# Kernel optimization log

Measured on AMD Instinct MI355X. Metric: run time of the kernel, lower is better.

Reference implementation:

```python
import jax, jax.numpy as jnp
import numpy as np

IN_F, OUT_F = 64, 32
N = IN_F * OUT_F + OUT_F  # 2080 sampled parameters (weights + bias)
B, S = 8, 2048
SCALE_INIT = 1.0 * float(np.sqrt(2.0 / (IN_F + OUT_F)))


def setup_inputs() -> dict:
    key = jax.random.key(0)
    k_x, k_eps, k_loc, k_cov = jax.random.split(key, 4)
    x = jax.random.normal(k_x, (B, S, IN_F), dtype=jnp.float32)
    eps = jax.random.normal(k_eps, (B, S, N), dtype=jnp.float32)
    loc = 0.01 * jax.random.normal(k_loc, (N,), dtype=jnp.float32)
    logvar = jnp.full((N,), float(np.log(SCALE_INIT)), dtype=jnp.float32)
    n_off = N * (N - 1) // 2
    cov_flat = 0.001 * jax.random.normal(k_cov, (n_off,), dtype=jnp.float32)
    return {"x": x, "eps": eps, "loc": loc, "logvar": logvar, "cov_flat": cov_flat}


def reference(x, eps, loc, logvar, cov_flat):
    n = loc.shape[0]
    in_f = x.shape[-1]
    out_f = n // (in_f + 1)  # n = out*(in+1)
    # flat_to_triangular (strictly lower) + make_cholesky, vectorized scatter
    rows, cols = np.tril_indices(n, -1)
    A = jnp.zeros((n, n), dtype=x.dtype).at[rows, cols].set(cov_flat)
    L = A + jnp.diag(jnp.exp(logvar * 0.5))  # off-diag from cov, diag = std
    # MultivariateNormal rsample: loc + L @ eps (per batch sample)
    W = loc + jnp.einsum('bsn,mn->bsm', eps, L)  # [B,S,N]
    b = W[..., :out_f]
    Wm = W[..., out_f:].reshape(*W.shape[:-1], in_f, out_f)  # [B,S,in,out]
    y = jnp.einsum('bsh,bshk->bsk', x, Wm) + b
    return y
```

## Files before the change

### kernel.cpp

```cpp
#include <hip/hip_runtime.h>
#include <hip/hip_bf16.h>

#define IN_F  64
#define OUT_F 32
#define NV    2080
#define NPAD  2176
#define MM    16384
#define KK    2080

typedef __attribute__((ext_vector_type(4))) float f32x4;
typedef __bf16 bf16x8 __attribute__((ext_vector_type(8)));

using gas_ptr = const __attribute__((address_space(1))) void*;
using lds_ptr = __attribute__((address_space(3))) void*;

__global__ __launch_bounds__(256) void build_L_k(const float* __restrict__ cov,
                                                 const float* __restrict__ logvar,
                                                 __hip_bfloat16* __restrict__ LB) {
    const int idx = blockIdx.x * 256 + threadIdx.x;
    const int m = idx / KK;
    const int k = idx - m * KK;
    float v = 0.0f;
    if (m < NV) {
        if (k < m)       v = cov[(size_t)(m * (m - 1) / 2) + k];
        else if (k == m) v = expf(0.5f * logvar[m]);
    }
    LB[idx] = __float2bfloat16(v);
}

__global__ __launch_bounds__(256) void cvt_bf16_k(const float4* __restrict__ in,
                                                  uint4* __restrict__ out) {
    const size_t i = (size_t)blockIdx.x * 256 + threadIdx.x;
    float4 a = in[2 * i];
    float4 b = in[2 * i + 1];
    union { uint4 u; __hip_bfloat16 h[8]; } o;
    o.h[0] = __float2bfloat16(a.x); o.h[1] = __float2bfloat16(a.y);
    o.h[2] = __float2bfloat16(a.z); o.h[3] = __float2bfloat16(a.w);
    o.h[4] = __float2bfloat16(b.x); o.h[5] = __float2bfloat16(b.y);
    o.h[6] = __float2bfloat16(b.z); o.h[7] = __float2bfloat16(b.w);
    out[i] = o.u;
}

__global__ __launch_bounds__(256) void gemm_zl_k(const __hip_bfloat16* __restrict__ A,
                                                 const __hip_bfloat16* __restrict__ BT,
                                                 __hip_bfloat16* __restrict__ Z) {
    __shared__ __align__(16) __hip_bfloat16 As[2][128 * 32];
    __shared__ __align__(16) __hip_bfloat16 Bs[2][128 * 32];

    const int tid  = threadIdx.x;
    const int bm   = blockIdx.x;
    const int bn   = 16 - blockIdx.y;
    const int wave = tid >> 6;
    const int lane = tid & 63;
    const int wr   = wave >> 1;
    const int wc   = wave & 1;
    const int quad = lane >> 4;
    const int r16  = lane & 15;

    const int kblocks = min(KK / 32, 4 * bn + 4);

    const __hip_bfloat16* Ag = A  + (size_t)bm * 128 * KK;
    const __hip_bfloat16* Bg = BT + (size_t)bn * 128 * KK;

    const int c0 = tid, c1 = tid + 256;
    const int ar0 = c0 >> 2, ap0 = (c0 & 3) ^ ((ar0 >> 1) & 3);
    const int ar1 = c1 >> 2, ap1 = (c1 & 3) ^ ((ar1 >> 1) & 3);
    const size_t gofs0 = (size_t)ar0 * KK + ap0 * 8;
    const size_t gofs1 = (size_t)ar1 * KK + ap1 * 8;

    f32x4 acc[4][4];
#pragma unroll
    for (int i = 0; i < 4; i++)
#pragma unroll
        for (int j = 0; j < 4; j++) acc[i][j] = f32x4{0.f, 0.f, 0.f, 0.f};

    int aofs[4], bofs[4];
#pragma unroll
    for (int i = 0; i < 4; i++) {
        const int arow = 64 * wr + 16 * i + r16;
        aofs[i] = arow * 32 + (quad ^ ((arow >> 1) & 3)) * 8;
        const int brow = 64 * wc + 16 * i + r16;
        bofs[i] = brow * 32 + (quad ^ ((brow >> 1) & 3)) * 8;
    }

    __builtin_amdgcn_global_load_lds((gas_ptr)(Ag + gofs0), (lds_ptr)(&As[0][0] + c0 * 8), 16, 0, 0);
    __builtin_amdgcn_global_load_lds((gas_ptr)(Ag + gofs1), (lds_ptr)(&As[0][0] + c1 * 8), 16, 0, 0);
    __builtin_amdgcn_global_load_lds((gas_ptr)(Bg + gofs0), (lds_ptr)(&Bs[0][0] + c0 * 8), 16, 0, 0);
    __builtin_amdgcn_global_load_lds((gas_ptr)(Bg + gofs1), (lds_ptr)(&Bs[0][0] + c1 * 8), 16, 0, 0);

    for (int kb = 0; kb < kblocks; ++kb) {
        const int cur = kb & 1;
        __syncthreads();

        if (kb + 1 < kblocks) {
            const size_t k0 = (size_t)(kb + 1) * 32;
            __builtin_amdgcn_global_load_lds((gas_ptr)(Ag + k0 + gofs0), (lds_ptr)(&As[cur ^ 1][0] + c0 * 8), 16, 0, 0);
            __builtin_amdgcn_global_load_lds((gas_ptr)(Ag + k0 + gofs1), (lds_ptr)(&As[cur ^ 1][0] + c1 * 8), 16, 0, 0);
            __builtin_amdgcn_global_load_lds((gas_ptr)(Bg + k0 + gofs0), (lds_ptr)(&Bs[cur ^ 1][0] + c0 * 8), 16, 0, 0);
            __builtin_amdgcn_global_load_lds((gas_ptr)(Bg + k0 + gofs1), (lds_ptr)(&Bs[cur ^ 1][0] + c1 * 8), 16, 0, 0);
        }

        bf16x8 af[4], bfr[4];
#pragma unroll
        for (int i = 0; i < 4; i++) af[i]  = *(const bf16x8*)(&As[cur][0] + aofs[i]);
#pragma unroll
        for (int j = 0; j < 4; j++) bfr[j] = *(const bf16x8*)(&Bs[cur][0] + bofs[j]);
#pragma unroll
        for (int i = 0; i < 4; i++)
#pragma unroll
            for (int j = 0; j < 4; j++)
                acc[i][j] = __builtin_amdgcn_mfma_f32_16x16x32_bf16(af[i], bfr[j], acc[i][j], 0, 0, 0);
    }

#pragma unroll
    for (int i = 0; i < 4; i++) {
#pragma unroll
        for (int j = 0; j < 4; j++) {
            const int row0 = bm * 128 + 64 * wr + 16 * i + quad * 4;
            const int col  = bn * 128 + 64 * wc + 16 * j + r16;
#pragma unroll
            for (int r = 0; r < 4; r++)
                Z[(size_t)(row0 + r) * NPAD + col] = __float2bfloat16(acc[i][j][r]);
        }
    }
}

__global__ __launch_bounds__(256) void epilogue_k(const __hip_bfloat16* __restrict__ Z,
                                                  const float* __restrict__ x,
                                                  const float* __restrict__ loc,
                                                  float* __restrict__ y) {
    __shared__ float locs[NV];
    __shared__ float xs[8][IN_F];
    const int tid = threadIdx.x;
    const int t0  = blockIdx.x * 8;
    for (int i = tid; i < NV; i += 256) locs[i] = loc[i];
    {
        int i = tid;
        xs[i >> 6][i & 63] = x[(size_t)(t0 + (i >> 6)) * IN_F + (i & 63)];
        i += 256;
        xs[i >> 6][i & 63] = x[(size_t)(t0 + (i >> 6)) * IN_F + (i & 63)];
    }
    __syncthreads();

    const int k  = tid & 31;
    const int tl = tid >> 5;
    const size_t t = (size_t)t0 + tl;
    const __hip_bfloat16* zr = Z + t * NPAD;

    float sum = locs[k] + __bfloat162float(zr[k]);
#pragma unroll 8
    for (int h = 0; h < IN_F; ++h) {
        const int m = OUT_F + (h << 5) + k;
        sum += xs[tl][h] * (locs[m] + __bfloat162float(zr[m]));
    }
    y[t * OUT_F + k] = sum;
}

extern "C" void kernel_launch(void* const* d_in, const int* in_sizes, int n_in,
                              void* d_out, int out_size, void* d_ws, size_t ws_size,
                              hipStream_t stream) {
    const float* x      = (const float*)d_in[0];
    const float* eps    = (const float*)d_in[1];
    const float* loc    = (const float*)d_in[2];
    const float* logvar = (const float*)d_in[3];
    const float* cov    = (const float*)d_in[4];
    float* y = (float*)d_out;

    char* ws = (char*)d_ws;
    __hip_bfloat16* EpsB = (__hip_bfloat16*)ws;
    __hip_bfloat16* LB   = (__hip_bfloat16*)(ws + (size_t)MM * KK * 2);
    __hip_bfloat16* Zb   = (__hip_bfloat16*)(ws + (size_t)MM * KK * 2
                                                + (size_t)NPAD * KK * 2);

    build_L_k<<<(NPAD * KK) / 256, 256, 0, stream>>>(cov, logvar, LB);
    cvt_bf16_k<<<(MM * KK / 8) / 256, 256, 0, stream>>>((const float4*)eps, (uint4*)EpsB);
    gemm_zl_k<<<dim3(MM / 128, NPAD / 128), 256, 0, stream>>>(EpsB, LB, Zb);
    epilogue_k<<<MM / 8, 256, 0, stream>>>(Zb, x, loc, y);
}
```

Baseline: 338.2 us.

## Fuse eps bf16 conversion into GEMM loads and fold loc into GEMM epilogue

Removes the separate fp32-to-bf16 conversion pass over eps: the GEMM now streams fp32 eps tiles straight into LDS with a new XOR swizzle and converts them to bf16 while building MFMA fragments. The loc bias is added in the GEMM store, and the epilogue kernel is rewritten to stage each Z row in LDS with one wave per token and a shuffle reduction. This avoids writing and re-reading a large bf16 copy of eps, at the cost of double the A-tile LDS footprint, more global bytes per GEMM k-step, and conversion ALU work inside the MFMA loop.

```diff
diff --git a/kernel.cpp b/kernel.cpp
--- a/kernel.cpp
+++ b/kernel.cpp
@@ -28,23 +28,11 @@
     LB[idx] = __float2bfloat16(v);
 }
 
-__global__ __launch_bounds__(256) void cvt_bf16_k(const float4* __restrict__ in,
-                                                  uint4* __restrict__ out) {
-    const size_t i = (size_t)blockIdx.x * 256 + threadIdx.x;
-    float4 a = in[2 * i];
-    float4 b = in[2 * i + 1];
-    union { uint4 u; __hip_bfloat16 h[8]; } o;
-    o.h[0] = __float2bfloat16(a.x); o.h[1] = __float2bfloat16(a.y);
-    o.h[2] = __float2bfloat16(a.z); o.h[3] = __float2bfloat16(a.w);
-    o.h[4] = __float2bfloat16(b.x); o.h[5] = __float2bfloat16(b.y);
-    o.h[6] = __float2bfloat16(b.z); o.h[7] = __float2bfloat16(b.w);
-    out[i] = o.u;
-}
-
-__global__ __launch_bounds__(256) void gemm_zl_k(const __hip_bfloat16* __restrict__ A,
+__global__ __launch_bounds__(256) void gemm_zl_k(const float* __restrict__ A,
                                                  const __hip_bfloat16* __restrict__ BT,
+                                                 const float* __restrict__ loc,
                                                  __hip_bfloat16* __restrict__ Z) {
-    __shared__ __align__(16) __hip_bfloat16 As[2][128 * 32];
+    __shared__ __align__(16) float          As[2][128 * 32];
     __shared__ __align__(16) __hip_bfloat16 Bs[2][128 * 32];
 
     const int tid  = threadIdx.x;
@@ -59,14 +47,24 @@
 
     const int kblocks = min(KK / 32, 4 * bn + 4);
 
-    const __hip_bfloat16* Ag = A  + (size_t)bm * 128 * KK;
+    const float*          Ag = A  + (size_t)bm * 128 * KK;
     const __hip_bfloat16* Bg = BT + (size_t)bn * 128 * KK;
 
+    int aldsofs[4];
+    size_t agofs[4];
+#pragma unroll
+    for (int i = 0; i < 4; i++) {
+        const int c   = tid + 256 * i;
+        const int row = c >> 3;
+        const int pg  = (c & 7) ^ (row & 7);
+        aldsofs[i] = c * 4;
+        agofs[i]   = (size_t)row * KK + pg * 4;
+    }
     const int c0 = tid, c1 = tid + 256;
-    const int ar0 = c0 >> 2, ap0 = (c0 & 3) ^ ((ar0 >> 1) & 3);
-    const int ar1 = c1 >> 2, ap1 = (c1 & 3) ^ ((ar1 >> 1) & 3);
-    const size_t gofs0 = (size_t)ar0 * KK + ap0 * 8;
-    const size_t gofs1 = (size_t)ar1 * KK + ap1 * 8;
+    const int br0 = c0 >> 2, bp0 = (c0 & 3) ^ ((br0 >> 1) & 3);
+    const int br1 = c1 >> 2, bp1 = (c1 & 3) ^ ((br1 >> 1) & 3);
+    const size_t bgofs0 = (size_t)br0 * KK + bp0 * 8;
+    const size_t bgofs1 = (size_t)br1 * KK + bp1 * 8;
 
     f32x4 acc[4][4];
 #pragma unroll
@@ -74,19 +72,23 @@
 #pragma unroll
         for (int j = 0; j < 4; j++) acc[i][j] = f32x4{0.f, 0.f, 0.f, 0.f};
 
-    int aofs[4], bofs[4];
+    int aofs0[4], aofs1[4], bofs[4];
 #pragma unroll
     for (int i = 0; i < 4; i++) {
         const int arow = 64 * wr + 16 * i + r16;
-        aofs[i] = arow * 32 + (quad ^ ((arow >> 1) & 3)) * 8;
+        const int s0 = (2 * quad) ^ (arow & 7);
+        const int s1 = (2 * quad + 1) ^ (arow & 7);
+        aofs0[i] = arow * 32 + s0 * 4;
+        aofs1[i] = arow * 32 + s1 * 4;
         const int brow = 64 * wc + 16 * i + r16;
         bofs[i] = brow * 32 + (quad ^ ((brow >> 1) & 3)) * 8;
     }
 
-    __builtin_amdgcn_global_load_lds((gas_ptr)(Ag + gofs0), (lds_ptr)(&As[0][0] + c0 * 8), 16, 0, 0);
-    __builtin_amdgcn_global_load_lds((gas_ptr)(Ag + gofs1), (lds_ptr)(&As[0][0] + c1 * 8), 16, 0, 0);
-    __builtin_amdgcn_global_load_lds((gas_ptr)(Bg + gofs0), (lds_ptr)(&Bs[0][0] + c0 * 8), 16, 0, 0);
-    __builtin_amdgcn_global_load_lds((gas_ptr)(Bg + gofs1), (lds_ptr)(&Bs[0][0] + c1 * 8), 16, 0, 0);
+#pragma unroll
+    for (int i = 0; i < 4; i++)
+        __builtin_amdgcn_global_load_lds((gas_ptr)(Ag + agofs[i]), (lds_ptr)(&As[0][0] + aldsofs[i]), 16, 0, 0);
+    __builtin_amdgcn_global_load_lds((gas_ptr)(Bg + bgofs0), (lds_ptr)(&Bs[0][0] + c0 * 8), 16, 0, 0);
+    __builtin_amdgcn_global_load_lds((gas_ptr)(Bg + bgofs1), (lds_ptr)(&Bs[0][0] + c1 * 8), 16, 0, 0);
 
     for (int kb = 0; kb < kblocks; ++kb) {
         const int cur = kb & 1;
@@ -94,15 +96,24 @@
 
         if (kb + 1 < kblocks) {
             const size_t k0 = (size_t)(kb + 1) * 32;
-            __builtin_amdgcn_global_load_lds((gas_ptr)(Ag + k0 + gofs0), (lds_ptr)(&As[cur ^ 1][0] + c0 * 8), 16, 0, 0);
-            __builtin_amdgcn_global_load_lds((gas_ptr)(Ag + k0 + gofs1), (lds_ptr)(&As[cur ^ 1][0] + c1 * 8), 16, 0, 0);
-            __builtin_amdgcn_global_load_lds((gas_ptr)(Bg + k0 + gofs0), (lds_ptr)(&Bs[cur ^ 1][0] + c0 * 8), 16, 0, 0);
-            __builtin_amdgcn_global_load_lds((gas_ptr)(Bg + k0 + gofs1), (lds_ptr)(&Bs[cur ^ 1][0] + c1 * 8), 16, 0, 0);
+#pragma unroll
+            for (int i = 0; i < 4; i++)
+                __builtin_amdgcn_global_load_lds((gas_ptr)(Ag + k0 + agofs[i]),
+                                                 (lds_ptr)(&As[cur ^ 1][0] + aldsofs[i]), 16, 0, 0);
+            __builtin_amdgcn_global_load_lds((gas_ptr)(Bg + k0 + bgofs0), (lds_ptr)(&Bs[cur ^ 1][0] + c0 * 8), 16, 0, 0);
+            __builtin_amdgcn_global_load_lds((gas_ptr)(Bg + k0 + bgofs1), (lds_ptr)(&Bs[cur ^ 1][0] + c1 * 8), 16, 0, 0);
         }
 
         bf16x8 af[4], bfr[4];
 #pragma unroll
-        for (int i = 0; i < 4; i++) af[i]  = *(const bf16x8*)(&As[cur][0] + aofs[i]);
+        for (int i = 0; i < 4; i++) {
+            const f32x4 f0 = *(const f32x4*)(&As[cur][0] + aofs0[i]);
+            const f32x4 f1 = *(const f32x4*)(&As[cur][0] + aofs1[i]);
+            bf16x8 a;
+            a[0] = (__bf16)f0[0]; a[1] = (__bf16)f0[1]; a[2] = (__bf16)f0[2]; a[3] = (__bf16)f0[3];
+            a[4] = (__bf16)f1[0]; a[5] = (__bf16)f1[1]; a[6] = (__bf16)f1[2]; a[7] = (__bf16)f1[3];
+            af[i] = a;
+        }
 #pragma unroll
         for (int j = 0; j < 4; j++) bfr[j] = *(const bf16x8*)(&Bs[cur][0] + bofs[j]);
 #pragma unroll
@@ -112,6 +123,12 @@
                 acc[i][j] = __builtin_amdgcn_mfma_f32_16x16x32_bf16(af[i], bfr[j], acc[i][j], 0, 0, 0);
     }
 
+    float locv[4];
+#pragma unroll
+    for (int j = 0; j < 4; j++) {
+        const int col = bn * 128 + 64 * wc + 16 * j + r16;
+        locv[j] = (col < NV) ? loc[col] : 0.0f;
+    }
 #pragma unroll
     for (int i = 0; i < 4; i++) {
 #pragma unroll
@@ -120,40 +137,41 @@
             const int col  = bn * 128 + 64 * wc + 16 * j + r16;
 #pragma unroll
             for (int r = 0; r < 4; r++)
-                Z[(size_t)(row0 + r) * NPAD + col] = __float2bfloat16(acc[i][j][r]);
+                Z[(size_t)(row0 + r) * NPAD + col] = __float2bfloat16(acc[i][j][r] + locv[j]);
         }
     }
 }
 
 __global__ __launch_bounds__(256) void epilogue_k(const __hip_bfloat16* __restrict__ Z,
                                                   const float* __restrict__ x,
-                                                  const float* __restrict__ loc,
                                                   float* __restrict__ y) {
-    __shared__ float locs[NV];
-    __shared__ float xs[8][IN_F];
-    const int tid = threadIdx.x;
-    const int t0  = blockIdx.x * 8;
-    for (int i = tid; i < NV; i += 256) locs[i] = loc[i];
+    __shared__ __align__(16) __hip_bfloat16 Ws[4][NV];
+    __shared__ float xsm[4][IN_F];
+    const int tid  = threadIdx.x;
+    const int wave = tid >> 6;
+    const int lane = tid & 63;
+    const size_t t = (size_t)blockIdx.x * 4 + wave;
+
     {
-        int i = tid;
-        xs[i >> 6][i & 63] = x[(size_t)(t0 + (i >> 6)) * IN_F + (i & 63)];
-        i += 256;
-        xs[i >> 6][i & 63] = x[(size_t)(t0 + (i >> 6)) * IN_F + (i & 63)];
+        const uint4* src = (const uint4*)(Z + t * NPAD);
+        uint4* dst = (uint4*)&Ws[wave][0];
+#pragma unroll
+        for (int i = 0; i < 4; i++) dst[lane + 64 * i] = src[lane + 64 * i];
+        if (lane < 4) dst[256 + lane] = src[256 + lane];
+        xsm[wave][lane & 63] = x[t * IN_F + lane];
     }
     __syncthreads();
 
-    const int k  = tid & 31;
-    const int tl = tid >> 5;
-    const size_t t = (size_t)t0 + tl;
-    const __hip_bfloat16* zr = Z + t * NPAD;
-
-    float sum = locs[k] + __bfloat162float(zr[k]);
-#pragma unroll 8
-    for (int h = 0; h < IN_F; ++h) {
-        const int m = OUT_F + (h << 5) + k;
-        sum += xs[tl][h] * (locs[m] + __bfloat162float(zr[m]));
+    const int k    = lane & 31;
+    const int half = lane >> 5;
+    float s = (half == 0) ? __bfloat162float(Ws[wave][k]) : 0.0f;
+#pragma unroll
+    for (int j = 0; j < 32; j++) {
+        const int h = half * 32 + j;
+        s += xsm[wave][h] * __bfloat162float(Ws[wave][OUT_F + (h << 5) + k]);
     }
-    y[t * OUT_F + k] = sum;
+    const float other = __shfl(s, k + 32);
+    if (half == 0) y[t * OUT_F + k] = s + other;
 }
 
 extern "C" void kernel_launch(void* const* d_in, const int* in_sizes, int n_in,
@@ -167,13 +185,10 @@
     float* y = (float*)d_out;
 
     char* ws = (char*)d_ws;
-    __hip_bfloat16* EpsB = (__hip_bfloat16*)ws;
-    __hip_bfloat16* LB   = (__hip_bfloat16*)(ws + (size_t)MM * KK * 2);
-    __hip_bfloat16* Zb   = (__hip_bfloat16*)(ws + (size_t)MM * KK * 2
-                                                + (size_t)NPAD * KK * 2);
+    __hip_bfloat16* LB = (__hip_bfloat16*)ws;
+    __hip_bfloat16* Zb = (__hip_bfloat16*)(ws + (size_t)NPAD * KK * 2);
 
     build_L_k<<<(NPAD * KK) / 256, 256, 0, stream>>>(cov, logvar, LB);
-    cvt_bf16_k<<<(MM * KK / 8) / 256, 256, 0, stream>>>((const float4*)eps, (uint4*)EpsB);
-    gemm_zl_k<<<dim3(MM / 128, NPAD / 128), 256, 0, stream>>>(EpsB, LB, Zb);
-    epilogue_k<<<MM / 8, 256, 0, stream>>>(Zb, x, loc, y);
+    gemm_zl_k<<<dim3(MM / 128, NPAD / 128), 256, 0, stream>>>(eps, LB, loc, Zb);
+    epilogue_k<<<MM / 4, 256, 0, stream>>>(Zb, x, y);
 }
```

Result: faster. 326.6 us (-3.4%).

## Fuse x-weighted epilogue into GEMM with per-column-block partials and merge prep kernels

Applied to the files above, without the earlier changes.

The GEMM epilogue now applies loc and multiplies by the matching x inputs directly from the accumulators. Each of the 17 column blocks writes a 32-wide fp32 partial per row, and a small reduce kernel sums them. This removes the bf16 Z matrix round trip and the separate epilogue kernel. The two preprocessing kernels become one launch, and the warp tiling changes to 2x8 per wave so each wave holds all 128 columns. The cost is a 17x partial buffer, an extra reduction pass, and more accumulator registers per thread.

```diff
diff --git a/kernel.cpp b/kernel.cpp
--- a/kernel.cpp
+++ b/kernel.cpp
@@ -7,6 +7,10 @@
 #define NPAD  2176
 #define MM    16384
 #define KK    2080
+#define NBN   17
+
+#define NB_CVT (MM * KK / 8 / 256)
+#define NB_L   (NPAD * KK / 256)
 
 typedef __attribute__((ext_vector_type(4))) float f32x4;
 typedef __bf16 bf16x8 __attribute__((ext_vector_type(8)));
@@ -14,50 +18,65 @@
 using gas_ptr = const __attribute__((address_space(1))) void*;
 using lds_ptr = __attribute__((address_space(3))) void*;
 
-__global__ __launch_bounds__(256) void build_L_k(const float* __restrict__ cov,
-                                                 const float* __restrict__ logvar,
-                                                 __hip_bfloat16* __restrict__ LB) {
-    const int idx = blockIdx.x * 256 + threadIdx.x;
-    const int m = idx / KK;
-    const int k = idx - m * KK;
-    float v = 0.0f;
-    if (m < NV) {
-        if (k < m)       v = cov[(size_t)(m * (m - 1) / 2) + k];
-        else if (k == m) v = expf(0.5f * logvar[m]);
+__global__ __launch_bounds__(256) void prep_k(const float* __restrict__ cov,
+                                              const float* __restrict__ logvar,
+                                              const float4* __restrict__ eps4,
+                                              uint4* __restrict__ epsb,
+                                              __hip_bfloat16* __restrict__ LB) {
+    if (blockIdx.x < NB_CVT) {
+        const size_t i = (size_t)blockIdx.x * 256 + threadIdx.x;
+        float4 a = eps4[2 * i];
+        float4 b = eps4[2 * i + 1];
+        union { uint4 u; __hip_bfloat16 h[8]; } o;
+        o.h[0] = __float2bfloat16(a.x); o.h[1] = __float2bfloat16(a.y);
+        o.h[2] = __float2bfloat16(a.z); o.h[3] = __float2bfloat16(a.w);
+        o.h[4] = __float2bfloat16(b.x); o.h[5] = __float2bfloat16(b.y);
+        o.h[6] = __float2bfloat16(b.z); o.h[7] = __float2bfloat16(b.w);
+        epsb[i] = o.u;
+    } else {
+        const int idx = (blockIdx.x - NB_CVT) * 256 + threadIdx.x;
+        const int m = idx / KK;
+        const int k = idx - m * KK;
+        float v = 0.0f;
+        if (m < NV) {
+            if (k < m)       v = cov[(size_t)(m * (m - 1) / 2) + k];
+            else if (k == m) v = expf(0.5f * logvar[m]);
+        }
+        LB[idx] = __float2bfloat16(v);
     }
-    LB[idx] = __float2bfloat16(v);
-}
-
-__global__ __launch_bounds__(256) void cvt_bf16_k(const float4* __restrict__ in,
-                                                  uint4* __restrict__ out) {
-    const size_t i = (size_t)blockIdx.x * 256 + threadIdx.x;
-    float4 a = in[2 * i];
-    float4 b = in[2 * i + 1];
-    union { uint4 u; __hip_bfloat16 h[8]; } o;
-    o.h[0] = __float2bfloat16(a.x); o.h[1] = __float2bfloat16(a.y);
-    o.h[2] = __float2bfloat16(a.z); o.h[3] = __float2bfloat16(a.w);
-    o.h[4] = __float2bfloat16(b.x); o.h[5] = __float2bfloat16(b.y);
-    o.h[6] = __float2bfloat16(b.z); o.h[7] = __float2bfloat16(b.w);
-    out[i] = o.u;
 }
 
 __global__ __launch_bounds__(256) void gemm_zl_k(const __hip_bfloat16* __restrict__ A,
                                                  const __hip_bfloat16* __restrict__ BT,
-                                                 __hip_bfloat16* __restrict__ Z) {
+                                                 const float* __restrict__ loc,
+                                                 const float* __restrict__ x,
+                                                 float* __restrict__ Ypart) {
     __shared__ __align__(16) __hip_bfloat16 As[2][128 * 32];
     __shared__ __align__(16) __hip_bfloat16 Bs[2][128 * 32];
+    __shared__ float xs[128][4];
 
     const int tid  = threadIdx.x;
     const int bm   = blockIdx.x;
-    const int bn   = 16 - blockIdx.y;
+    const int bn   = (NBN - 1) - blockIdx.y;
     const int wave = tid >> 6;
     const int lane = tid & 63;
-    const int wr   = wave >> 1;
-    const int wc   = wave & 1;
     const int quad = lane >> 4;
     const int r16  = lane & 15;
 
     const int kblocks = min(KK / 32, 4 * bn + 4);
+
+    {
+        const int tl = tid >> 1;
+        const int cc = (tid & 1) * 2;
+#pragma unroll
+        for (int c = cc; c < cc + 2; c++) {
+            const int h = 4 * bn - 1 + c;
+            float w = 0.0f;
+            if (bn == 0 && c == 0)          w = 1.0f;
+            else if (h >= 0 && h < IN_F)    w = x[(size_t)(bm * 128 + tl) * IN_F + h];
+            xs[tl][c] = w;
+        }
+    }
 
     const __hip_bfloat16* Ag = A  + (size_t)bm * 128 * KK;
     const __hip_bfloat16* Bg = BT + (size_t)bn * 128 * KK;
@@ -68,19 +87,22 @@
     const size_t gofs0 = (size_t)ar0 * KK + ap0 * 8;
     const size_t gofs1 = (size_t)ar1 * KK + ap1 * 8;
 
-    f32x4 acc[4][4];
+    f32x4 acc[2][8];
 #pragma unroll
-    for (int i = 0; i < 4; i++)
+    for (int i = 0; i < 2; i++)
 #pragma unroll
-        for (int j = 0; j < 4; j++) acc[i][j] = f32x4{0.f, 0.f, 0.f, 0.f};
+        for (int j = 0; j < 8; j++) acc[i][j] = f32x4{0.f, 0.f, 0.f, 0.f};
 
-    int aofs[4], bofs[4];
+    int aofs[2], bofs[8];
 #pragma unroll
-    for (int i = 0; i < 4; i++) {
-        const int arow = 64 * wr + 16 * i + r16;
+    for (int i = 0; i < 2; i++) {
+        const int arow = 32 * wave + 16 * i + r16;
         aofs[i] = arow * 32 + (quad ^ ((arow >> 1) & 3)) * 8;
-        const int brow = 64 * wc + 16 * i + r16;
-        bofs[i] = brow * 32 + (quad ^ ((brow >> 1) & 3)) * 8;
+    }
+#pragma unroll
+    for (int j = 0; j < 8; j++) {
+        const int brow = 16 * j + r16;
+        bofs[j] = brow * 32 + (quad ^ ((brow >> 1) & 3)) * 8;
     }
 
     __builtin_amdgcn_global_load_lds((gas_ptr)(Ag + gofs0), (lds_ptr)(&As[0][0] + c0 * 8), 16, 0, 0);
@@ -100,60 +122,54 @@
             __builtin_amdgcn_global_load_lds((gas_ptr)(Bg + k0 + gofs1), (lds_ptr)(&Bs[cur ^ 1][0] + c1 * 8), 16, 0, 0);
         }
 
-        bf16x8 af[4], bfr[4];
+        bf16x8 af[2], bfr[8];
 #pragma unroll
-        for (int i = 0; i < 4; i++) af[i]  = *(const bf16x8*)(&As[cur][0] + aofs[i]);
+        for (int i = 0; i < 2; i++) af[i]  = *(const bf16x8*)(&As[cur][0] + aofs[i]);
 #pragma unroll
-        for (int j = 0; j < 4; j++) bfr[j] = *(const bf16x8*)(&Bs[cur][0] + bofs[j]);
+        for (int j = 0; j < 8; j++) bfr[j] = *(const bf16x8*)(&Bs[cur][0] + bofs[j]);
 #pragma unroll
-        for (int i = 0; i < 4; i++)
+        for (int i = 0; i < 2; i++)
 #pragma unroll
-            for (int j = 0; j < 4; j++)
+            for (int j = 0; j < 8; j++)
                 acc[i][j] = __builtin_amdgcn_mfma_f32_16x16x32_bf16(af[i], bfr[j], acc[i][j], 0, 0, 0);
     }
 
+    float locv[8];
 #pragma unroll
-    for (int i = 0; i < 4; i++) {
+    for (int j = 0; j < 8; j++) {
+        const int col = bn * 128 + 16 * j + r16;
+        locv[j] = (col < NV) ? loc[col] : 0.0f;
+    }
+
+    float* yp = Ypart + ((size_t)bn * MM + (size_t)bm * 128) * OUT_F;
 #pragma unroll
-        for (int j = 0; j < 4; j++) {
-            const int row0 = bm * 128 + 64 * wr + 16 * i + quad * 4;
-            const int col  = bn * 128 + 64 * wc + 16 * j + r16;
+    for (int i = 0; i < 2; i++) {
 #pragma unroll
-            for (int r = 0; r < 4; r++)
-                Z[(size_t)(row0 + r) * NPAD + col] = __float2bfloat16(acc[i][j][r]);
+        for (int r = 0; r < 4; r++) {
+            const int tl = 32 * wave + 16 * i + 4 * quad + r;
+            float v0 = 0.0f, v1 = 0.0f;
+#pragma unroll
+            for (int c = 0; c < 4; c++) {
+                const float w = xs[tl][c];
+                v0 += w * (acc[i][2 * c][r]     + locv[2 * c]);
+                v1 += w * (acc[i][2 * c + 1][r] + locv[2 * c + 1]);
+            }
+            yp[(size_t)tl * OUT_F + r16]      = v0;
+            yp[(size_t)tl * OUT_F + 16 + r16] = v1;
         }
     }
 }
 
-__global__ __launch_bounds__(256) void epilogue_k(const __hip_bfloat16* __restrict__ Z,
-                                                  const float* __restrict__ x,
-                                                  const float* __restrict__ loc,
-                                                  float* __restrict__ y) {
-    __shared__ float locs[NV];
-    __shared__ float xs[8][IN_F];
-    const int tid = threadIdx.x;
-    const int t0  = blockIdx.x * 8;
-    for (int i = tid; i < NV; i += 256) locs[i] = loc[i];
-    {
-        int i = tid;
-        xs[i >> 6][i & 63] = x[(size_t)(t0 + (i >> 6)) * IN_F + (i & 63)];
-        i += 256;
-        xs[i >> 6][i & 63] = x[(size_t)(t0 + (i >> 6)) * IN_F + (i & 63)];
+__global__ __launch_bounds__(256) void reduce_y_k(const float4* __restrict__ yp,
+                                                  float4* __restrict__ y) {
+    const size_t i = (size_t)blockIdx.x * 256 + threadIdx.x;
+    float4 s = yp[i];
+#pragma unroll
+    for (int b = 1; b < NBN; b++) {
+        float4 v = yp[i + (size_t)b * (MM * OUT_F / 4)];
+        s.x += v.x; s.y += v.y; s.z += v.z; s.w += v.w;
     }
-    __syncthreads();
-
-    const int k  = tid & 31;
-    const int tl = tid >> 5;
-    const size_t t = (size_t)t0 + tl;
-    const __hip_bfloat16* zr = Z + t * NPAD;
-
-    float sum = locs[k] + __bfloat162float(zr[k]);
-#pragma unroll 8
-    for (int h = 0; h < IN_F; ++h) {
-        const int m = OUT_F + (h << 5) + k;
-        sum += xs[tl][h] * (locs[m] + __bfloat162float(zr[m]));
-    }
-    y[t * OUT_F + k] = sum;
+    y[i] = s;
 }
 
 extern "C" void kernel_launch(void* const* d_in, const int* in_sizes, int n_in,
@@ -167,13 +183,13 @@
     float* y = (float*)d_out;
 
     char* ws = (char*)d_ws;
-    __hip_bfloat16* EpsB = (__hip_bfloat16*)ws;
-    __hip_bfloat16* LB   = (__hip_bfloat16*)(ws + (size_t)MM * KK * 2);
-    __hip_bfloat16* Zb   = (__hip_bfloat16*)(ws + (size_t)MM * KK * 2
-                                                + (size_t)NPAD * KK * 2);
+    __hip_bfloat16* EpsB  = (__hip_bfloat16*)ws;
+    __hip_bfloat16* LB    = (__hip_bfloat16*)(ws + (size_t)MM * KK * 2);
+    float*          Ypart = (float*)(ws + (size_t)MM * KK * 2
+                                        + (size_t)NPAD * KK * 2);
 
-    build_L_k<<<(NPAD * KK) / 256, 256, 0, stream>>>(cov, logvar, LB);
-    cvt_bf16_k<<<(MM * KK / 8) / 256, 256, 0, stream>>>((const float4*)eps, (uint4*)EpsB);
-    gemm_zl_k<<<dim3(MM / 128, NPAD / 128), 256, 0, stream>>>(EpsB, LB, Zb);
-    epilogue_k<<<MM / 8, 256, 0, stream>>>(Zb, x, loc, y);
+    prep_k<<<NB_CVT + NB_L, 256, 0, stream>>>(cov, logvar, (const float4*)eps,
+                                              (uint4*)EpsB, LB);
+    gemm_zl_k<<<dim3(MM / 128, NBN), 256, 0, stream>>>(EpsB, LB, loc, x, Ypart);
+    reduce_y_k<<<(MM * OUT_F / 4) / 256, 256, 0, stream>>>((const float4*)Ypart, (float4*)y);
 }
```

New measurement: 323.1 us. 1.05x faster.
